# Kernel optimization log

Measured on AMD Instinct MI355X. Metric: run time of the kernel, lower is better.

## Reference

```python
import jax, jax.numpy as jnp
import numpy as np

NH, NP, MA, FL = 8, 4, 2, 3   # heads, points, max_num_agent, feature_level
L = MA * FL                    # total sampling levels = 6
C = 256
BS, NQ = 8, 4096
SS = np.array([[64, 64], [32, 32], [16, 16]] * MA, dtype=np.int64)  # [L,2] (H,W)
NV = int((SS[:, 0] * SS[:, 1]).sum())  # 10752


def setup_inputs() -> dict:
    key = jax.random.key(0)
    ks = jax.random.split(key, 8)
    f32 = jnp.float32
    return {
        'query': jax.random.normal(ks[0], (BS, NQ, C), f32),
        'query_pos': jax.random.normal(ks[1], (BS, NQ, C), f32),
        'value': jax.random.normal(ks[2], (BS, NV, C), f32),
        'reference_points': jax.random.uniform(ks[3], (BS, NQ, L, 2), f32),
        'spatial_shapes': SS,
        'W_off': jax.random.normal(ks[4], (C, L * NH * NP * 2), f32) * 0.01,
        'b_off': jnp.zeros((L * NH * NP * 2,), f32),
        'W_attn': jax.random.normal(ks[5], (C, L * NH * NP), f32) * 0.05,
        'b_attn': jnp.zeros((L * NH * NP,), f32),
        'W_val': jax.random.normal(ks[6], (C, C), f32) * 0.05,
        'b_val': jnp.zeros((C,), f32),
        'W_out': jax.random.normal(ks[7], (C, C), f32) * 0.05,
        'b_out': jnp.zeros((C,), f32),
    }


def _ms_deform_attn(v, loc, attn, ss):
    # v: [bs, nv, NH, d]; loc: [bs, nq, NH, L, NP, 2] in [0,1] (x,y)
    # attn: [bs, nq, NH, L, NP]; ss: np int array [L,2] (H,W) -- static
    bs, nq = loc.shape[0], loc.shape[1]
    d = v.shape[-1]
    starts = np.concatenate([[0], np.cumsum(ss[:, 0] * ss[:, 1])[:-1]])
    out = jnp.zeros((bs, NH, nq, d), v.dtype)
    for l in range(L):
        H, W = int(ss[l, 0]), int(ss[l, 1])
        s0 = int(starts[l])
        vl = v[:, s0:s0 + H * W].transpose(0, 2, 1, 3)  # [bs, NH, HW, d]
        # sampling coords, grid_sample align_corners=False convention
        x = loc[:, :, :, l, :, 0].transpose(0, 2, 1, 3) * W - 0.5  # [bs,NH,nq,NP]
        y = loc[:, :, :, l, :, 1].transpose(0, 2, 1, 3) * H - 0.5
        x0 = jnp.floor(x); y0 = jnp.floor(y)
        lx = x - x0; ly = y - y0
        x0i = x0.astype(jnp.int32); y0i = y0.astype(jnp.int32)

        def gather(yi, xi):
            valid = (yi >= 0) & (yi < H) & (xi >= 0) & (xi < W)
            idx = jnp.clip(yi, 0, H - 1) * W + jnp.clip(xi, 0, W - 1)  # [bs,NH,nq,NP]
            g = jnp.take_along_axis(vl, idx.reshape(bs, NH, nq * NP, 1), axis=2)
            g = g.reshape(bs, NH, nq, NP, d)
            return g * valid[..., None].astype(g.dtype)  # zero padding outside

        sampled = ((1 - lx) * (1 - ly))[..., None] * gather(y0i, x0i) \
                + (lx * (1 - ly))[..., None] * gather(y0i, x0i + 1) \
                + ((1 - lx) * ly)[..., None] * gather(y0i + 1, x0i) \
                + (lx * ly)[..., None] * gather(y0i + 1, x0i + 1)
        aw = attn[:, :, :, l, :].transpose(0, 2, 1, 3)  # [bs,NH,nq,NP]
        out = out + jnp.einsum('bhqpd,bhqp->bhqd', sampled, aw)
    return out.transpose(0, 2, 1, 3).reshape(bs, nq, NH * d)


def reference(query, query_pos, value, reference_points, spatial_shapes,
              W_off, b_off, W_attn, b_attn, W_val, b_val, W_out, b_out):
    ss = np.asarray(spatial_shapes)
    identity = query
    q = query + query_pos
    bs, nv, c = value.shape
    nq = q.shape[1]
    v = (value @ W_val + b_val).reshape(bs, nv, NH, c // NH)
    off = (q @ W_off + b_off).reshape(bs, nq, NH, L, NP, 2)
    attn = (q @ W_attn + b_attn).reshape(bs, nq, NH, L * NP)
    attn = jax.nn.softmax(attn, axis=-1).reshape(bs, nq, NH, L, NP)
    offset_normalizer = jnp.asarray(np.stack([ss[:, 1], ss[:, 0]], -1), q.dtype)  # [L,2] (W,H)
    loc = reference_points[:, :, None, :, None, :] \
        + off / offset_normalizer[None, None, None, :, None, :]
    out = _ms_deform_attn(v, loc, attn, ss)
    out = out @ W_out + b_out
    return out + identity  # dropout is identity in eval mode
```

## Files before the change

kernel.cpp:

```cpp
#include <hip/hip_runtime.h>

#define NHEAD 8
#define NPOINT 4
#define NLVL 6
#define CDIM 256
#define BSZ 8
#define NQRY 4096
#define NVAL 10752

typedef __attribute__((ext_vector_type(8))) short short8;
typedef __attribute__((ext_vector_type(4))) float floatx4;
typedef __attribute__((ext_vector_type(2))) float float2v;

__device__ __forceinline__ unsigned short f2bf(float f) {
    unsigned u = __float_as_uint(f);
    return (unsigned short)((u + 0x7FFFu + ((u >> 16) & 1u)) >> 16);
}
__device__ __forceinline__ unsigned pack2(float a, float b) {
    return (unsigned)f2bf(a) | ((unsigned)f2bf(b) << 16);
}
__device__ __forceinline__ float blo(unsigned u) { return __uint_as_float(u << 16); }
__device__ __forceinline__ float bhi(unsigned u) { return __uint_as_float(u & 0xffff0000u); }

__global__ __launch_bounds__(256) void prep_w(
    const float* __restrict__ Wv, const float* __restrict__ Woff,
    const float* __restrict__ Wattn, const float* __restrict__ Wo,
    unsigned short* __restrict__ Wt)
{
    const int id = blockIdx.x * 256 + threadIdx.x;
    const int n = id >> 8, k = id & 255;
    float val;
    if (n < 256) val = Wv[k * 256 + n];
    else if (n < 832) {
        const int nn = n - 256;
        val = (nn < 384) ? Woff[k * 384 + nn] : Wattn[k * 192 + (nn - 384)];
    } else val = Wo[k * 256 + (n - 832)];
    Wt[id] = f2bf(val);
}

__global__ __launch_bounds__(256) void q_conv(
    const float* __restrict__ query, const float* __restrict__ qpos,
    unsigned short* __restrict__ qbf)
{
    const long i = ((long)blockIdx.x * 256 + threadIdx.x) * 4;
    const float4 a = *(const float4*)(query + i);
    const float4 b = *(const float4*)(qpos + i);
    ushort4 r;
    r.x = f2bf(a.x + b.x); r.y = f2bf(a.y + b.y);
    r.z = f2bf(a.z + b.z); r.w = f2bf(a.w + b.w);
    *(ushort4*)(qbf + i) = r;
}

template<int BN, int ABF, int VTRANS, int RESID, int SPLITB>
__global__ __launch_bounds__(512) void gemm_mfma(
    const void* __restrict__ Av, const unsigned short* __restrict__ Bt,
    const float* __restrict__ bias, const float* __restrict__ bias2,
    const float* __restrict__ resid, void* __restrict__ Cv,
    int M, int Ntot)
{
    constexpr int BK = 32, BMt = 128, PAD = 8;
    constexpr int WN = BN / 4, NT = WN / 16;
    __shared__ unsigned short As[BMt][BK + PAD];
    __shared__ unsigned short Bs[BN][BK + PAD];
    const int tid = threadIdx.x;
    const int bm = blockIdx.y * BMt;
    const int bcol = blockIdx.x * BN;
    const int wid = tid >> 6, lane = tid & 63;
    const int wm = (wid >> 2) * 64, wn = (wid & 3) * WN;
    const int lm = lane & 15, q8 = (lane >> 4) * 8;

    floatx4 acc[4][NT];
#pragma unroll
    for (int i = 0; i < 4; ++i)
#pragma unroll
        for (int j = 0; j < NT; ++j) acc[i][j] = (floatx4)0.0f;

    const int arow = tid >> 2, akp = (tid & 3) * 8;
    const int bn_ = tid >> 1, bkp = (tid & 1) * 16;

    for (int k0 = 0; k0 < 256; k0 += BK) {
        if (ABF) {
            const unsigned short* A = (const unsigned short*)Av;
            uint4 v = *(const uint4*)(A + (long)(bm + arow) * 256 + k0 + akp);
            *(uint4*)&As[arow][akp] = v;
        } else {
            const float* A = (const float*)Av;
            const float* p = A + (long)(bm + arow) * 256 + k0 + akp;
            const float4 a = *(const float4*)p;
            const float4 b = *(const float4*)(p + 4);
            uint4 v;
            v.x = pack2(a.x, a.y); v.y = pack2(a.z, a.w);
            v.z = pack2(b.x, b.y); v.w = pack2(b.z, b.w);
            *(uint4*)&As[arow][akp] = v;
        }
        if (bn_ < BN) {
            const unsigned short* p = Bt + (long)(bcol + bn_) * 256 + k0 + bkp;
            uint4 v0 = *(const uint4*)p;
            uint4 v1 = *(const uint4*)(p + 8);
            *(uint4*)&Bs[bn_][bkp] = v0;
            *(uint4*)&Bs[bn_][bkp + 8] = v1;
        }
        __syncthreads();
        short8 af[4], bfr[NT];
#pragma unroll
        for (int i = 0; i < 4; ++i) af[i] = *(const short8*)&As[wm + i * 16 + lm][q8];
#pragma unroll
        for (int j = 0; j < NT; ++j) bfr[j] = *(const short8*)&Bs[wn + j * 16 + lm][q8];
#pragma unroll
        for (int i = 0; i < 4; ++i)
#pragma unroll
            for (int j = 0; j < NT; ++j)
                acc[i][j] = __builtin_amdgcn_mfma_f32_16x16x32_bf16(af[i], bfr[j], acc[i][j], 0, 0, 0);
        __syncthreads();
    }

    const int qrow = (lane >> 4) * 4;
#pragma unroll
    for (int j = 0; j < NT; ++j) {
        const int colg = bcol + wn + j * 16 + lm;
        const float bv = (SPLITB && colg >= 384) ? bias2[colg - 384] : bias[colg];
#pragma unroll
        for (int i = 0; i < 4; ++i) {
#pragma unroll
            for (int r = 0; r < 4; ++r) {
                const int rowl = wm + i * 16 + qrow + r;
                const int rowg = bm + rowl;
                float val = acc[i][j][r] + bv;
                if (VTRANS) {
                    const int b = bm / NVAL;
                    const int pos = bm - b * NVAL + rowl;
                    const int h = colg >> 5, d = colg & 31;
                    ((unsigned short*)Cv)[(((long)(b * NHEAD + h)) * NVAL + pos) * 32 + d] = f2bf(val);
                } else {
                    if (RESID) val += resid[(long)rowg * 256 + colg];
                    ((float*)Cv)[(long)rowg * Ntot + colg] = val;
                }
            }
        }
    }
}

__global__ __launch_bounds__(256) void ms_sample4(
    const unsigned short* __restrict__ v,
    const float* __restrict__ oa,
    const float* __restrict__ refp,
    unsigned short* __restrict__ outi)
{
    __shared__ float s_rec[4][192 * 6];
    __shared__ float s_ref[4][12];
    const int tid = threadIdx.x;
    const int w = tid >> 6;
    const int lane = tid & 63;
    const int bq = blockIdx.x * 4 + w;
    const int b = bq >> 12;

    if (lane < 12) s_ref[w][lane] = refp[(long)bq * 12 + lane];
    __syncthreads();

    const int h = lane >> 3;
    const int li = lane & 7;
    const float* oarow = oa + (long)bq * 576;

    const float* lgp = oarow + 384 + h * 24 + li * 3;
    const float lg0 = lgp[0], lg1 = lgp[1], lg2 = lgp[2];
    float mx = fmaxf(lg0, fmaxf(lg1, lg2));
    mx = fmaxf(mx, __shfl_xor(mx, 1));
    mx = fmaxf(mx, __shfl_xor(mx, 2));
    mx = fmaxf(mx, __shfl_xor(mx, 4));
    const float e0 = __expf(lg0 - mx);
    const float e1 = __expf(lg1 - mx);
    const float e2 = __expf(lg2 - mx);
    float den = e0 + e1 + e2;
    den += __shfl_xor(den, 1);
    den += __shfl_xor(den, 2);
    den += __shfl_xor(den, 4);
    const float inv = 1.0f / den;
    const float aw_[3] = {e0 * inv, e1 * inv, e2 * inv};

    const float* offp = oarow + (h * 24 + li * 3) * 2;
    const float2v od0 = *(const float2v*)(offp);
    const float2v od1 = *(const float2v*)(offp + 2);
    const float2v od2 = *(const float2v*)(offp + 4);

#pragma unroll
    for (int k = 0; k < 3; ++k) {
        const int lp = li * 3 + k;
        const int l = lp >> 2;
        const int sh = (l >= 3) ? (l - 3) : l;
        const int W = 64 >> sh;
        const int base = ((l >= 3) ? 5376 : 0)
                       + ((sh >= 1) ? 4096 : 0)
                       + ((sh >= 2) ? 1024 : 0);
        const float Wf = (float)W;
        const float ox = (k == 0) ? od0.x : (k == 1) ? od1.x : od2.x;
        const float oy = (k == 0) ? od0.y : (k == 1) ? od1.y : od2.y;
        const float rx = s_ref[w][l * 2 + 0];
        const float ry = s_ref[w][l * 2 + 1];
        const float x = rx * Wf + ox - 0.5f;
        const float y = ry * Wf + oy - 0.5f;
        const float xf = floorf(x), yf = floorf(y);
        const int x0 = (int)xf, y0 = (int)yf;
        const float lx = x - xf, ly = y - yf;
        const float wx0 = (x0 >= 0 && x0 < W)      ? (1.f - lx) : 0.f;
        const float wx1 = (x0 >= -1 && x0 < W - 1) ? lx         : 0.f;
        const float wy0 = (y0 >= 0 && y0 < W)      ? (1.f - ly) : 0.f;
        const float wy1 = (y0 >= -1 && y0 < W - 1) ? ly         : 0.f;
        const int y0c = min(max(y0, 0), W - 1);
        const int y1c = min(max(y0 + 1, 0), W - 1);
        const int xb = min(max(x0, 0), W - 2);
        const float wl = (xb == x0) ? wx0 : ((xb == x0 + 1) ? wx1 : 0.f);
        const float wr = (xb == x0) ? wx1 : ((xb == x0 - 1) ? wx0 : 0.f);
        const float aw = aw_[k];
        const float awl = aw * wl, awr = aw * wr;
        float* r = &s_rec[w][((lp << 3) + h) * 6];
        float2v wlv, wrv;
        wlv.x = awl * wy0; wlv.y = awl * wy1;
        wrv.x = awr * wy0; wrv.y = awr * wy1;
        *(float2v*)(r)     = wlv;
        *(float2v*)(r + 2) = wrv;
        uint2 pk;
        pk.x = (unsigned)(base + y0c * W + xb) * 64u;
        pk.y = (unsigned)(base + y1c * W + xb) * 64u;
        *(uint2*)(r + 4) = pk;
    }
    __syncthreads();

    const unsigned lane_base =
        (unsigned)((b * NHEAD + h) * NVAL) * 64u + (unsigned)li * 16u;
    const char* vbase = (const char*)v;
    const int sel = (li >> 2) * 2;
    const float* rp0 = &s_rec[w][h * 6];
    float2v a01 = {0.f, 0.f}, a23 = {0.f, 0.f};
    float2v a45 = {0.f, 0.f}, a67 = {0.f, 0.f};

#pragma unroll 8
    for (int lp = 0; lp < NLVL * NPOINT; ++lp) {
        const float* rp = rp0 + lp * 48;
        const float2v wv = *(const float2v*)(rp + sel);
        const uint2 off = *(const uint2*)(rp + 4);
        const uint4 u0 = *(const uint4*)(vbase + (lane_base + off.x));
        const uint4 u1 = *(const uint4*)(vbase + (lane_base + off.y));
        float2v c;
        c.x = blo(u0.x); c.y = bhi(u0.x); a01 += wv.x * c;
        c.x = blo(u0.y); c.y = bhi(u0.y); a23 += wv.x * c;
        c.x = blo(u0.z); c.y = bhi(u0.z); a45 += wv.x * c;
        c.x = blo(u0.w); c.y = bhi(u0.w); a67 += wv.x * c;
        c.x = blo(u1.x); c.y = bhi(u1.x); a01 += wv.y * c;
        c.x = blo(u1.y); c.y = bhi(u1.y); a23 += wv.y * c;
        c.x = blo(u1.z); c.y = bhi(u1.z); a45 += wv.y * c;
        c.x = blo(u1.w); c.y = bhi(u1.w); a67 += wv.y * c;
    }

    a01.x += __shfl_xor(a01.x, 4); a01.y += __shfl_xor(a01.y, 4);
    a23.x += __shfl_xor(a23.x, 4); a23.y += __shfl_xor(a23.y, 4);
    a45.x += __shfl_xor(a45.x, 4); a45.y += __shfl_xor(a45.y, 4);
    a67.x += __shfl_xor(a67.x, 4); a67.y += __shfl_xor(a67.y, 4);

    const int hi = li >> 2;
    const float o0 = hi ? a45.x : a01.x;
    const float o1 = hi ? a45.y : a01.y;
    const float o2 = hi ? a67.x : a23.x;
    const float o3 = hi ? a67.y : a23.y;
    ushort4 o;
    o.x = f2bf(o0); o.y = f2bf(o1); o.z = f2bf(o2); o.w = f2bf(o3);
    const int d = (li & 3) * 8 + hi * 4;
    *(ushort4*)(outi + (long)bq * CDIM + h * 32 + d) = o;
}

extern "C" void kernel_launch(void* const* d_in, const int* in_sizes, int n_in,
                              void* d_out, int out_size, void* d_ws, size_t ws_size,
                              hipStream_t stream) {
    const float* query     = (const float*)d_in[0];
    const float* query_pos = (const float*)d_in[1];
    const float* value     = (const float*)d_in[2];
    const float* refp      = (const float*)d_in[3];
    const float* W_off  = (const float*)d_in[5];
    const float* b_off  = (const float*)d_in[6];
    const float* W_attn = (const float*)d_in[7];
    const float* b_attn = (const float*)d_in[8];
    const float* W_val  = (const float*)d_in[9];
    const float* b_val  = (const float*)d_in[10];
    const float* W_out  = (const float*)d_in[11];
    const float* b_out  = (const float*)d_in[12];
    float* out = (float*)d_out;

    unsigned short* v_bf = (unsigned short*)d_ws;
    unsigned short* q_bf = v_bf + (long)86016 * 256;
    unsigned short* Wt   = q_bf + (long)32768 * 256;
    float* oa_ws = (float*)(Wt + (long)1088 * 256);
    unsigned short* i_bf = (unsigned short*)(oa_ws + (long)32768 * 576);

    const int MV = BSZ * NVAL;
    const int MQ = BSZ * NQRY;

    prep_w<<<1088, 256, 0, stream>>>(W_val, W_off, W_attn, W_out, Wt);
    q_conv<<<(MQ * CDIM / 4) / 256, 256, 0, stream>>>(query, query_pos, q_bf);
    gemm_mfma<256, 0, 1, 0, 0><<<dim3(1, MV / 128), 512, 0, stream>>>(
        value, Wt, b_val, nullptr, nullptr, v_bf, MV, 256);
    gemm_mfma<192, 1, 0, 0, 1><<<dim3(3, MQ / 128), 512, 0, stream>>>(
        q_bf, Wt + (long)256 * 256, b_off, b_attn, nullptr, oa_ws, MQ, 576);
    ms_sample4<<<MQ / 4, 256, 0, stream>>>(v_bf, oa_ws, refp, i_bf);
    gemm_mfma<256, 1, 0, 1, 0><<<dim3(1, MQ / 128), 512, 0, stream>>>(
        i_bf, Wt + (long)832 * 256, b_out, nullptr, query, out, MQ, 256);
}
```

Measured before the change: 394.0 us.

## Use direct global-to-LDS loads with XOR-swizzled layout and BK=64 in GEMM

Reworks the MFMA GEMM tile loading: operands are copied straight from global memory into LDS with global_load_lds, skipping the register round trip. The padded 2D LDS arrays become an XOR-swizzled flat buffer, which avoids bank conflicts without padding. The K tile grows from 32 to 64, so there are fewer barriers per output tile. The price is more LDS per block, and the fp32 A path still converts through registers.

```diff
diff --git a/kernel.cpp b/kernel.cpp
--- a/kernel.cpp
+++ b/kernel.cpp
@@ -21,6 +21,12 @@
 }
 __device__ __forceinline__ float blo(unsigned u) { return __uint_as_float(u << 16); }
 __device__ __forceinline__ float bhi(unsigned u) { return __uint_as_float(u & 0xffff0000u); }
+
+__device__ __forceinline__ void gload16(const void* g, void* l) {
+    __builtin_amdgcn_global_load_lds(
+        (const __attribute__((address_space(1))) unsigned int*)g,
+        (__attribute__((address_space(3))) unsigned int*)l, 16, 0, 0);
+}
 
 __global__ __launch_bounds__(256) void prep_w(
     const float* __restrict__ Wv, const float* __restrict__ Woff,
@@ -58,59 +64,90 @@
     const float* __restrict__ resid, void* __restrict__ Cv,
     int M, int Ntot)
 {
-    constexpr int BK = 32, BMt = 128, PAD = 8;
+    constexpr int BK = 64, BMt = 128;
     constexpr int WN = BN / 4, NT = WN / 16;
-    __shared__ unsigned short As[BMt][BK + PAD];
-    __shared__ unsigned short Bs[BN][BK + PAD];
+    constexpr int ACH = BMt * (BK / 8);
+    constexpr int BCH = BN * (BK / 8);
+    constexpr int NCH = ACH + BCH;
+    __shared__ char smem[NCH * 16];
     const int tid = threadIdx.x;
     const int bm = blockIdx.y * BMt;
     const int bcol = blockIdx.x * BN;
     const int wid = tid >> 6, lane = tid & 63;
     const int wm = (wid >> 2) * 64, wn = (wid & 3) * WN;
-    const int lm = lane & 15, q8 = (lane >> 4) * 8;
+    const int lm = lane & 15;
 
     floatx4 acc[4][NT];
 #pragma unroll
     for (int i = 0; i < 4; ++i)
 #pragma unroll
         for (int j = 0; j < NT; ++j) acc[i][j] = (floatx4)0.0f;
-
-    const int arow = tid >> 2, akp = (tid & 3) * 8;
-    const int bn_ = tid >> 1, bkp = (tid & 1) * 16;
 
     for (int k0 = 0; k0 < 256; k0 += BK) {
         if (ABF) {
             const unsigned short* A = (const unsigned short*)Av;
-            uint4 v = *(const uint4*)(A + (long)(bm + arow) * 256 + k0 + akp);
-            *(uint4*)&As[arow][akp] = v;
+            constexpr int NI = NCH / 512;
+#pragma unroll
+            for (int j = 0; j < NI; ++j) {
+                const int cbase = (wid * NI + j) * 64;
+                const int g = cbase + lane;
+                const unsigned short* src;
+                if (cbase < ACH) {
+                    const int row = g >> 3, c = (g & 7) ^ (row & 7);
+                    src = A + (long)(bm + row) * 256 + k0 + c * 8;
+                } else {
+                    const int g2 = g - ACH;
+                    const int row = g2 >> 3, c = (g2 & 7) ^ (row & 7);
+                    src = Bt + (long)(bcol + row) * 256 + k0 + c * 8;
+                }
+                gload16(src, smem + cbase * 16);
+            }
         } else {
+            constexpr int NIB = BCH / 512;
+#pragma unroll
+            for (int j = 0; j < NIB; ++j) {
+                const int cbase = (wid * NIB + j) * 64;
+                const int g2 = cbase + lane;
+                const int row = g2 >> 3, c = (g2 & 7) ^ (row & 7);
+                gload16(Bt + (long)(bcol + row) * 256 + k0 + c * 8,
+                        smem + ACH * 16 + cbase * 16);
+            }
             const float* A = (const float*)Av;
-            const float* p = A + (long)(bm + arow) * 256 + k0 + akp;
-            const float4 a = *(const float4*)p;
-            const float4 b = *(const float4*)(p + 4);
-            uint4 v;
-            v.x = pack2(a.x, a.y); v.y = pack2(a.z, a.w);
-            v.z = pack2(b.x, b.y); v.w = pack2(b.z, b.w);
-            *(uint4*)&As[arow][akp] = v;
-        }
-        if (bn_ < BN) {
-            const unsigned short* p = Bt + (long)(bcol + bn_) * 256 + k0 + bkp;
-            uint4 v0 = *(const uint4*)p;
-            uint4 v1 = *(const uint4*)(p + 8);
-            *(uint4*)&Bs[bn_][bkp] = v0;
-            *(uint4*)&Bs[bn_][bkp + 8] = v1;
+#pragma unroll
+            for (int j = 0; j < 2; ++j) {
+                const int g = j * 512 + tid;
+                const int row = g >> 3, c = g & 7;
+                const float* p = A + (long)(bm + row) * 256 + k0 + c * 8;
+                const float4 a = *(const float4*)p;
+                const float4 b = *(const float4*)(p + 4);
+                uint4 v;
+                v.x = pack2(a.x, a.y); v.y = pack2(a.z, a.w);
+                v.z = pack2(b.x, b.y); v.w = pack2(b.z, b.w);
+                *(uint4*)(smem + row * 128 + ((c ^ (row & 7)) << 4)) = v;
+            }
         }
         __syncthreads();
-        short8 af[4], bfr[NT];
-#pragma unroll
-        for (int i = 0; i < 4; ++i) af[i] = *(const short8*)&As[wm + i * 16 + lm][q8];
-#pragma unroll
-        for (int j = 0; j < NT; ++j) bfr[j] = *(const short8*)&Bs[wn + j * 16 + lm][q8];
-#pragma unroll
-        for (int i = 0; i < 4; ++i)
-#pragma unroll
-            for (int j = 0; j < NT; ++j)
-                acc[i][j] = __builtin_amdgcn_mfma_f32_16x16x32_bf16(af[i], bfr[j], acc[i][j], 0, 0, 0);
+
+#pragma unroll
+        for (int kk = 0; kk < 2; ++kk) {
+            const int cc = kk * 4 + (lane >> 4);
+            short8 af[4], bfr[NT];
+#pragma unroll
+            for (int i = 0; i < 4; ++i) {
+                const int row = wm + i * 16 + lm;
+                af[i] = *(const short8*)(smem + row * 128 + ((cc ^ (row & 7)) << 4));
+            }
+#pragma unroll
+            for (int j = 0; j < NT; ++j) {
+                const int row = wn + j * 16 + lm;
+                bfr[j] = *(const short8*)(smem + ACH * 16 + row * 128 + ((cc ^ (row & 7)) << 4));
+            }
+#pragma unroll
+            for (int i = 0; i < 4; ++i)
+#pragma unroll
+                for (int j = 0; j < NT; ++j)
+                    acc[i][j] = __builtin_amdgcn_mfma_f32_16x16x32_bf16(af[i], bfr[j], acc[i][j], 0, 0, 0);
+        }
         __syncthreads();
     }
 
```

New measurement: 366.7 us. 6.9% less time.
